# Kernel optimization log

Hardware: AMD Instinct MI355X
Metric: run time of the kernel (lower is better)

## Reference

```python
import jax, jax.numpy as jnp
import numpy as np

N = 100000   # num nodes
E = 1600000  # num edges
D = 64       # feature / hidden dim (irreps_in == hidden_dim)
SCALE = D ** -0.5


def setup_inputs() -> dict:
    key = jax.random.key(0)
    ks = jax.random.split(key, 6)
    x = jax.random.normal(ks[0], (N, D), dtype=jnp.float32)
    edge_index = jax.random.randint(ks[1], (2, E), 0, N, dtype=jnp.int32)
    std = D ** -0.5
    Wq = jax.random.normal(ks[2], (D, D), dtype=jnp.float32) * std
    Wk = jax.random.normal(ks[3], (D, D), dtype=jnp.float32) * std
    Wv = jax.random.normal(ks[4], (D, D), dtype=jnp.float32) * std
    Wo = jax.random.normal(ks[5], (D, D), dtype=jnp.float32) * std
    return {"x": x, "edge_index": edge_index, "Wq": Wq, "Wk": Wk, "Wv": Wv, "Wo": Wo}


def reference(x, edge_index, Wq, Wk, Wv, Wo):
    # Per-receiver variable-length attention over incoming neighbors.
    # Mathematically identical to the torch module's degree-bucketed SDPA
    # (softmax over each node's neighbor set), without padding buffers.
    sender, receiver = edge_index[0], edge_index[1]
    Q = x @ Wq  # [N, D]
    K = x @ Wk
    V = x @ Wv
    # per-edge logits: <Q[receiver], K[sender]> * scale
    s = jnp.einsum('ed,ed->e', Q[receiver], K[sender]) * SCALE  # [E]
    # numerically stable segment softmax over receiver groups
    m = jax.ops.segment_max(s, receiver, num_segments=N)  # -inf for empty segments
    m_safe = jnp.where(jnp.isfinite(m), m, 0.0)
    p = jnp.exp(s - m_safe[receiver])  # [E]
    denom = jax.ops.segment_sum(p, receiver, num_segments=N)  # [N]
    num = jax.ops.segment_sum(p[:, None] * V[sender], receiver, num_segments=N)  # [N, D]
    # zero-degree nodes get out = 0 (matches torch: skipped buckets + nan_to_num)
    out = jnp.where(denom[:, None] > 0,
                    num / jnp.maximum(denom, 1e-30)[:, None],
                    0.0)
    return x + out @ Wo
```

## Files before the change

kernel.cpp:

```cpp
#include <hip/hip_runtime.h>
#include <hip/hip_bf16.h>

#define DIM 64
#define SCALE 0.125f
#define BINSH 5
#define NPB 32
#define BCAP 768
#define CHUNK 8192
#define MAXBINS 3200

static __device__ __forceinline__ unsigned int pack2bf(float a, float b) {
    unsigned int ua = __float_as_uint(a), ub = __float_as_uint(b);
    ua += 0x7fffu + ((ua >> 16) & 1u);
    ub += 0x7fffu + ((ub >> 16) & 1u);
    return (ua >> 16) | (ub & 0xffff0000u);
}
static __device__ __forceinline__ float2 unpack2bf(unsigned int u) {
    return make_float2(__uint_as_float(u << 16), __uint_as_float(u & 0xffff0000u));
}

__global__ __launch_bounds__(256) void k_wmul(const float* __restrict__ Wv,
                                              const float* __restrict__ Wo,
                                              float* __restrict__ Wvo) {
    __shared__ __align__(16) float av[64 * 64];
    __shared__ __align__(16) float bo[64 * 64];
    int tid = threadIdx.x;
    for (int i = tid; i < 1024; i += 256) {
        ((float4*)av)[i] = ((const float4*)Wv)[i];
        ((float4*)bo)[i] = ((const float4*)Wo)[i];
    }
    __syncthreads();
    int r = tid >> 2, c0 = (tid & 3) * 16;
    float acc[16];
#pragma unroll
    for (int j = 0; j < 16; j++) acc[j] = 0.f;
    for (int k = 0; k < 64; k++) {
        float a = av[r * 64 + k];
#pragma unroll
        for (int j = 0; j < 16; j++)
            acc[j] = fmaf(a, bo[k * 64 + c0 + j], acc[j]);
    }
#pragma unroll
    for (int j = 0; j < 16; j++) Wvo[r * 64 + c0 + j] = acc[j];
}

__global__ __launch_bounds__(256) void k_fused(const int* __restrict__ send,
                                               const int* __restrict__ recv,
                                               const float* __restrict__ x,
                                               const float* __restrict__ Wq,
                                               const float* __restrict__ Wk,
                                               const float* __restrict__ Wvo,
                                               int* __restrict__ binCur,
                                               unsigned int* __restrict__ ebufA,
                                               float* __restrict__ Q,
                                               unsigned int* __restrict__ KVb,
                                               int E, int N, int NBK,
                                               int NBIN, int nchunk) {
    __shared__ __align__(16) float smem[16384];
    int tid = threadIdx.x;

    if ((int)blockIdx.x < NBIN) {
        int* hist = (int*)smem;
        int* lcur = hist + MAXBINS;
        int base = blockIdx.x * CHUNK;
        int lim = min(base + CHUNK, E);

        for (int i = tid; i < NBK; i += 256) hist[i] = 0;
        __syncthreads();
        for (int i = base + tid; i < lim; i += 256)
            atomicAdd(&hist[recv[i] >> BINSH], 1);
        __syncthreads();
        for (int i = tid; i < NBK; i += 256) {
            int h = hist[i];
            lcur[i] = h ? atomicAdd(&binCur[i], h) : 0;
        }
        __syncthreads();
        for (int i = base + tid; i < lim; i += 256) {
            int r = recv[i];
            int b = r >> BINSH;
            int p = atomicAdd(&lcur[b], 1);
            if (p < BCAP)
                ebufA[(size_t)b * BCAP + p] =
                    (unsigned)send[i] | ((unsigned)(r & (NPB - 1)) << 17);
        }
        return;
    }

    int wv = tid >> 6;
    int lane = tid & 63;
    int qb = blockIdx.x - NBIN;
    int m = qb / nchunk;
    int cb = qb % nchunk;
    const float* W = (m == 0) ? Wq : ((m == 1) ? Wk : Wvo);

    int base = cb * 256 + wv * 64;
    if (base < N) {
        float* xw = smem + wv * 4096;
#pragma unroll
        for (int c4 = 0; c4 < 16; c4++) {
            float4 v = make_float4(0.f, 0.f, 0.f, 0.f);
            if (base + lane < N) v = ((const float4*)x)[(size_t)(base + lane) * 16 + c4];
            xw[(c4 * 4 + 0) * 64 + lane] = v.x;
            xw[(c4 * 4 + 1) * 64 + lane] = v.y;
            xw[(c4 * 4 + 2) * 64 + lane] = v.z;
            xw[(c4 * 4 + 3) * 64 + lane] = v.w;
        }
        asm volatile("s_waitcnt lgkmcnt(0)" ::: "memory");

        int lr = lane >> 3;
        int lc = lane & 7;
        const float* xp = xw + lr * 8;
        const float* wp = W + lc * 8;

        float acc[8][8];
#pragma unroll
        for (int i = 0; i < 8; i++)
#pragma unroll
            for (int j = 0; j < 8; j++) acc[i][j] = 0.f;

        float4 xa = *(const float4*)(xp);
        float4 xb = *(const float4*)(xp + 4);
        float4 wa0 = *(const float4*)(wp);
        float4 wb0 = *(const float4*)(wp + 4);
        float4 wa1 = *(const float4*)(wp + 64);
        float4 wb1 = *(const float4*)(wp + 68);
#pragma unroll 4
        for (int k = 0; k < 64; k++) {
            float4 xan, xbn, wan, wbn;
            if (k < 63) {
                xan = *(const float4*)(xp + (k + 1) * 64);
                xbn = *(const float4*)(xp + (k + 1) * 64 + 4);
            }
            if (k < 62) {
                wan = *(const float4*)(wp + (k + 2) * 64);
                wbn = *(const float4*)(wp + (k + 2) * 64 + 4);
            }
            float xv[8] = {xa.x, xa.y, xa.z, xa.w, xb.x, xb.y, xb.z, xb.w};
            float wc[8] = {wa0.x, wa0.y, wa0.z, wa0.w, wb0.x, wb0.y, wb0.z, wb0.w};
#pragma unroll
            for (int i = 0; i < 8; i++)
#pragma unroll
                for (int j = 0; j < 8; j++)
                    acc[i][j] = fmaf(xv[i], wc[j], acc[i][j]);
            xa = xan; xb = xbn;
            wa0 = wa1; wb0 = wb1;
            wa1 = wan; wb1 = wbn;
        }

#pragma unroll
        for (int i = 0; i < 8; i++) {
            int row = base + lr * 8 + i;
            if (row < N) {
                if (m == 0) {
                    float* dst = &Q[(size_t)row * 64 + lc * 8];
                    ((float4*)dst)[0] = make_float4(acc[i][0], acc[i][1], acc[i][2], acc[i][3]);
                    ((float4*)dst)[1] = make_float4(acc[i][4], acc[i][5], acc[i][6], acc[i][7]);
                } else {
                    unsigned int* dst = &KVb[(size_t)row * 64 + (m - 1) * 32 + lc * 4];
                    uint4 pk;
                    pk.x = pack2bf(acc[i][0], acc[i][1]);
                    pk.y = pack2bf(acc[i][2], acc[i][3]);
                    pk.z = pack2bf(acc[i][4], acc[i][5]);
                    pk.w = pack2bf(acc[i][6], acc[i][7]);
                    *((uint4*)dst) = pk;
                }
            }
        }
    }
}

__global__ __launch_bounds__(256) void k_attn(const float* __restrict__ Q,
                                              const unsigned int* __restrict__ KVb,
                                              const float* __restrict__ x,
                                              const int* __restrict__ binCur,
                                              const unsigned int* __restrict__ ebufA,
                                              float* __restrict__ out, int N) {
    __shared__ unsigned int llist[BCAP];
    __shared__ int ldeg[NPB], lofs[NPB + 1], lcur[NPB];
    int tid = threadIdx.x;
    int wv = tid >> 6;
    int lane = tid & 63;
    int g = lane >> 3;
    int sub = lane & 7;

    int j = blockIdx.x;
    int cnt = min(binCur[j], BCAP);
    const unsigned int* ebin = ebufA + (size_t)j * BCAP;

    if (tid < NPB) ldeg[tid] = 0;
    __syncthreads();

    for (int i = tid; i < cnt; i += 256)
        atomicAdd(&ldeg[(ebin[i] >> 17) & (NPB - 1)], 1);
    __syncthreads();

    if (wv == 0 && lane < NPB) {
        int d = ldeg[lane];
        int s = d;
        for (int o = 1; o < NPB; o <<= 1) {
            int t = __shfl_up(s, o, NPB);
            if ((lane & (NPB - 1)) >= o) s += t;
        }
        lofs[lane + 1] = s;
        lcur[lane] = s - d;
        if (lane == 0) lofs[0] = 0;
    }
    __syncthreads();

    for (int i = tid; i < cnt; i += 256) {
        unsigned int u = ebin[i];
        int n = (u >> 17) & (NPB - 1);
        int p = atomicAdd(&lcur[n], 1);
        llist[p] = u & 0x1FFFFu;
    }
    __syncthreads();

    for (int n = wv; n < NPB; n += 4) {
        int r = (j << BINSH) + n;
        if (r >= N) break;
        int start = lofs[n];
        int end = lofs[n + 1];
        float4 qa = *((const float4*)&Q[(size_t)r * 64 + sub * 8]);
        float4 qb = *((const float4*)&Q[(size_t)r * 64 + sub * 8 + 4]);
        float q[8] = {qa.x, qa.y, qa.z, qa.w, qb.x, qb.y, qb.z, qb.w};
        float acc[8] = {0.f, 0.f, 0.f, 0.f, 0.f, 0.f, 0.f, 0.f};
        float dpart = 0.f;

        int eA = start + g;
        bool vA = eA < end;
        unsigned int sA = vA ? llist[eA] : 0u;
        uint4 kA = *((const uint4*)&KVb[(size_t)sA * 64 + sub * 4]);
        uint4 uA = *((const uint4*)&KVb[(size_t)sA * 64 + 32 + sub * 4]);
        int eB = start + 8 + g;
        bool vB = eB < end;
        unsigned int sB = vB ? llist[eB] : 0u;
        uint4 kB = *((const uint4*)&KVb[(size_t)sB * 64 + sub * 4]);
        uint4 uB = *((const uint4*)&KVb[(size_t)sB * 64 + 32 + sub * 4]);

        for (int bb = start; bb < end; bb += 8) {
            int eC = bb + 16 + g;
            bool vC = eC < end;
            unsigned int sC = vC ? llist[eC] : 0u;
            uint4 kC = *((const uint4*)&KVb[(size_t)sC * 64 + sub * 4]);
            uint4 uC = *((const uint4*)&KVb[(size_t)sC * 64 + 32 + sub * 4]);

            float2 k01 = unpack2bf(kA.x), k23 = unpack2bf(kA.y);
            float2 k45 = unpack2bf(kA.z), k67 = unpack2bf(kA.w);
            float dot = q[0] * k01.x + q[1] * k01.y + q[2] * k23.x + q[3] * k23.y
                      + q[4] * k45.x + q[5] * k45.y + q[6] * k67.x + q[7] * k67.y;
            dot += __shfl_xor(dot, 1);
            dot += __shfl_xor(dot, 2);
            dot += __shfl_xor(dot, 4);
            float w = vA ? __expf(dot * SCALE) : 0.f;

            float2 v01 = unpack2bf(uA.x), v23 = unpack2bf(uA.y);
            float2 v45 = unpack2bf(uA.z), v67 = unpack2bf(uA.w);
            acc[0] = fmaf(w, v01.x, acc[0]);
            acc[1] = fmaf(w, v01.y, acc[1]);
            acc[2] = fmaf(w, v23.x, acc[2]);
            acc[3] = fmaf(w, v23.y, acc[3]);
            acc[4] = fmaf(w, v45.x, acc[4]);
            acc[5] = fmaf(w, v45.y, acc[5]);
            acc[6] = fmaf(w, v67.x, acc[6]);
            acc[7] = fmaf(w, v67.y, acc[7]);
            dpart += w;

            kA = kB; uA = uB; vA = vB;
            kB = kC; uB = uC; vB = vC;
        }

        dpart += __shfl_xor(dpart, 8); dpart += __shfl_xor(dpart, 16); dpart += __shfl_xor(dpart, 32);
#pragma unroll
        for (int jj = 0; jj < 8; jj++) {
            acc[jj] += __shfl_xor(acc[jj], 8);
            acc[jj] += __shfl_xor(acc[jj], 16);
            acc[jj] += __shfl_xor(acc[jj], 32);
        }

        float inv = (dpart > 0.f) ? (1.0f / dpart) : 0.f;

        if (g == 0) {
            float4 xa = *((const float4*)&x[(size_t)r * 64 + sub * 8]);
            float4 xb = *((const float4*)&x[(size_t)r * 64 + sub * 8 + 4]);
            float4 oa = make_float4(fmaf(acc[0], inv, xa.x), fmaf(acc[1], inv, xa.y),
                                    fmaf(acc[2], inv, xa.z), fmaf(acc[3], inv, xa.w));
            float4 ob = make_float4(fmaf(acc[4], inv, xb.x), fmaf(acc[5], inv, xb.y),
                                    fmaf(acc[6], inv, xb.z), fmaf(acc[7], inv, xb.w));
            *((float4*)&out[(size_t)r * 64 + sub * 8]) = oa;
            *((float4*)&out[(size_t)r * 64 + sub * 8 + 4]) = ob;
        }
    }
}


extern "C" void kernel_launch(void* const* d_in, const int* in_sizes, int n_in,
                              void* d_out, int out_size, void* d_ws, size_t ws_size,
                              hipStream_t stream) {
    const float* x  = (const float*)d_in[0];
    const int* edge = (const int*)d_in[1];
    const float* Wq = (const float*)d_in[2];
    const float* Wk = (const float*)d_in[3];
    const float* Wv = (const float*)d_in[4];
    const float* Wo = (const float*)d_in[5];
    float* out = (float*)d_out;

    int N = in_sizes[0] / DIM;
    int E = in_sizes[1] / 2;
    int NBK = (N + NPB - 1) >> BINSH;

    char* p = (char*)d_ws;
    auto cv = [&](size_t bytes) {
        char* r = p;
        p += ((bytes + 255) / 256) * 256;
        return r;
    };
    float*        Q      = (float*)cv((size_t)N * 64 * 4);
    unsigned int* KVb    = (unsigned int*)cv((size_t)N * 64 * 4);
    float*        Wvo    = (float*)cv(64 * 64 * 4);
    int*          binCur = (int*)cv((size_t)NBK * 4);
    unsigned int* ebufA  = (unsigned int*)cv((size_t)NBK * BCAP * 4);
    (void)ws_size; (void)n_in; (void)out_size;

    const int* send = edge;
    const int* recv = edge + E;

    int NBIN = (E + CHUNK - 1) / CHUNK;
    int nchunk = (N + 255) / 256;

    hipMemsetAsync(binCur, 0, (size_t)NBK * 4, stream);
    k_wmul<<<1, 256, 0, stream>>>(Wv, Wo, Wvo);
    k_fused<<<NBIN + 3 * nchunk, 256, 0, stream>>>(send, recv, x, Wq, Wk, Wvo,
                                                   binCur, ebufA, Q, KVb,
                                                   E, N, NBK, NBIN, nchunk);
    k_attn<<<NBK, 256, 0, stream>>>(Q, KVb, x, binCur, ebufA, out, N);
}
```

Measured before the change: 231.1 us.

## Restructure edge binning into coarse buckets with a separate per-node CSR pass

```diff
diff --git a/kernel.cpp b/kernel.cpp
--- a/kernel.cpp
+++ b/kernel.cpp
@@ -6,8 +6,11 @@
 #define BINSH 5
 #define NPB 32
 #define BCAP 768
-#define CHUNK 8192
-#define MAXBINS 3200
+#define DBSH 8
+#define NDB 256
+#define CBCAP 4864
+#define CHUNKA 16384
+#define MAXCB 512
 
 static __device__ __forceinline__ unsigned int pack2bf(float a, float b) {
     unsigned int ua = __float_as_uint(a), ub = __float_as_uint(b);
@@ -19,98 +22,131 @@
     return make_float2(__uint_as_float(u << 16), __uint_as_float(u & 0xffff0000u));
 }
 
-__global__ __launch_bounds__(256) void k_wmul(const float* __restrict__ Wv,
-                                              const float* __restrict__ Wo,
-                                              float* __restrict__ Wvo) {
-    __shared__ __align__(16) float av[64 * 64];
-    __shared__ __align__(16) float bo[64 * 64];
+__global__ __launch_bounds__(1024) void k_prepA(const int* __restrict__ send,
+                                                const int* __restrict__ recv,
+                                                const float* __restrict__ Wv,
+                                                const float* __restrict__ Wo,
+                                                float* __restrict__ Wvo,
+                                                int* __restrict__ bucketCur,
+                                                unsigned int* __restrict__ cbuf,
+                                                int E, int NCB) {
+    __shared__ __align__(16) float smem[8192];
+    int* hist = (int*)smem;
+    int* lcur = hist + MAXCB;
     int tid = threadIdx.x;
-    for (int i = tid; i < 1024; i += 256) {
-        ((float4*)av)[i] = ((const float4*)Wv)[i];
-        ((float4*)bo)[i] = ((const float4*)Wo)[i];
-    }
-    __syncthreads();
-    int r = tid >> 2, c0 = (tid & 3) * 16;
-    float acc[16];
-#pragma unroll
-    for (int j = 0; j < 16; j++) acc[j] = 0.f;
-    for (int k = 0; k < 64; k++) {
-        float a = av[r * 64 + k];
-#pragma unroll
-        for (int j = 0; j < 16; j++)
-            acc[j] = fmaf(a, bo[k * 64 + c0 + j], acc[j]);
-    }
-#pragma unroll
-    for (int j = 0; j < 16; j++) Wvo[r * 64 + c0 + j] = acc[j];
-}
-
-__global__ __launch_bounds__(256) void k_fused(const int* __restrict__ send,
-                                               const int* __restrict__ recv,
-                                               const float* __restrict__ x,
+
+    if (blockIdx.x == 0) {
+        float* av = smem;
+        float* bo = smem + 4096;
+        ((float4*)av)[tid] = ((const float4*)Wv)[tid];
+        ((float4*)bo)[tid] = ((const float4*)Wo)[tid];
+        __syncthreads();
+        int r = tid >> 4, c0 = (tid & 15) * 4;
+        float acc[4] = {0.f, 0.f, 0.f, 0.f};
+        for (int k = 0; k < 64; k++) {
+            float a = av[r * 64 + k];
+#pragma unroll
+            for (int j = 0; j < 4; j++) acc[j] = fmaf(a, bo[k * 64 + c0 + j], acc[j]);
+        }
+#pragma unroll
+        for (int j = 0; j < 4; j++) Wvo[r * 64 + c0 + j] = acc[j];
+        __syncthreads();
+    }
+
+    int base = blockIdx.x * CHUNKA;
+    int lim = min(base + CHUNKA, E);
+
+    for (int i = tid; i < NCB; i += 1024) hist[i] = 0;
+    __syncthreads();
+    for (int i = base + tid; i < lim; i += 1024)
+        atomicAdd(&hist[recv[i] >> DBSH], 1);
+    __syncthreads();
+    for (int i = tid; i < NCB; i += 1024) {
+        int h = hist[i];
+        lcur[i] = h ? atomicAdd(&bucketCur[i], h) : 0;
+    }
+    __syncthreads();
+    for (int i = base + tid; i < lim; i += 1024) {
+        int r = recv[i];
+        int b = r >> DBSH;
+        int p = atomicAdd(&lcur[b], 1);
+        if (p < CBCAP)
+            cbuf[(size_t)b * CBCAP + p] =
+                (unsigned)send[i] | ((unsigned)(r & (NDB - 1)) << 17);
+    }
+}
+
+__global__ __launch_bounds__(256) void k_fused(const float* __restrict__ x,
                                                const float* __restrict__ Wq,
                                                const float* __restrict__ Wk,
                                                const float* __restrict__ Wvo,
-                                               int* __restrict__ binCur,
-                                               unsigned int* __restrict__ ebufA,
+                                               const int* __restrict__ bucketCur,
+                                               unsigned int* __restrict__ cbuf,
+                                               int* __restrict__ nstart,
+                                               int* __restrict__ ncount,
                                                float* __restrict__ Q,
                                                unsigned int* __restrict__ KVb,
-                                               int E, int N, int NBK,
-                                               int NBIN, int nchunk) {
-    __shared__ __align__(16) float smem[16384];
+                                               int N, int NCB, int nchunk) {
+    __shared__ __align__(16) float smem[8192];
     int tid = threadIdx.x;
-
-    if ((int)blockIdx.x < NBIN) {
-        int* hist = (int*)smem;
-        int* lcur = hist + MAXBINS;
-        int base = blockIdx.x * CHUNK;
-        int lim = min(base + CHUNK, E);
-
-        for (int i = tid; i < NBK; i += 256) hist[i] = 0;
-        __syncthreads();
-        for (int i = base + tid; i < lim; i += 256)
-            atomicAdd(&hist[recv[i] >> BINSH], 1);
-        __syncthreads();
-        for (int i = tid; i < NBK; i += 256) {
-            int h = hist[i];
-            lcur[i] = h ? atomicAdd(&binCur[i], h) : 0;
-        }
-        __syncthreads();
-        for (int i = base + tid; i < lim; i += 256) {
-            int r = recv[i];
-            int b = r >> BINSH;
-            int p = atomicAdd(&lcur[b], 1);
-            if (p < BCAP)
-                ebufA[(size_t)b * BCAP + p] =
-                    (unsigned)send[i] | ((unsigned)(r & (NPB - 1)) << 17);
-        }
-        return;
-    }
-
     int wv = tid >> 6;
     int lane = tid & 63;
-    int qb = blockIdx.x - NBIN;
+
+    if ((int)blockIdx.x < NCB) {
+        int b = blockIdx.x;
+        int bbase = b * CBCAP;
+        int cnt = min(bucketCur[b], CBCAP);
+        unsigned int* elist = (unsigned int*)smem;
+        int* ldeg = (int*)smem + CBCAP;
+        int* lcur = ldeg + NDB;
+        int* wsum = lcur + NDB;
+
+        for (int i = tid; i < cnt; i += 256) elist[i] = cbuf[bbase + i];
+        ldeg[tid] = 0;
+        __syncthreads();
+        for (int i = tid; i < cnt; i += 256)
+            atomicAdd(&ldeg[(elist[i] >> 17) & (NDB - 1)], 1);
+        __syncthreads();
+
+        int d = ldeg[tid];
+        int incl = d;
+        for (int o = 1; o < 64; o <<= 1) {
+            int t = __shfl_up(incl, o, 64);
+            if (lane >= o) incl += t;
+        }
+        if (lane == 63) wsum[wv] = incl;
+        __syncthreads();
+        int woff = 0;
+        for (int w2 = 0; w2 < wv; w2++) woff += wsum[w2];
+        int start = woff + incl - d;
+        lcur[tid] = start;
+        int r = (b << DBSH) + tid;
+        if (r < N) {
+            nstart[r] = bbase + start;
+            ncount[r] = d;
+        }
+        __syncthreads();
+
+        for (int i = tid; i < cnt; i += 256) {
+            unsigned u = elist[i];
+            int n = (u >> 17) & (NDB - 1);
+            int p = atomicAdd(&lcur[n], 1);
+            cbuf[bbase + p] = u & 0x1FFFFu;
+        }
+        return;
+    }
+
+    int qb = blockIdx.x - NCB;
     int m = qb / nchunk;
     int cb = qb % nchunk;
     const float* W = (m == 0) ? Wq : ((m == 1) ? Wk : Wvo);
 
     int base = cb * 256 + wv * 64;
     if (base < N) {
-        float* xw = smem + wv * 4096;
-#pragma unroll
-        for (int c4 = 0; c4 < 16; c4++) {
-            float4 v = make_float4(0.f, 0.f, 0.f, 0.f);
-            if (base + lane < N) v = ((const float4*)x)[(size_t)(base + lane) * 16 + c4];
-            xw[(c4 * 4 + 0) * 64 + lane] = v.x;
-            xw[(c4 * 4 + 1) * 64 + lane] = v.y;
-            xw[(c4 * 4 + 2) * 64 + lane] = v.z;
-            xw[(c4 * 4 + 3) * 64 + lane] = v.w;
-        }
-        asm volatile("s_waitcnt lgkmcnt(0)" ::: "memory");
-
+        float* xw = smem + wv * 2048;
         int lr = lane >> 3;
         int lc = lane & 7;
         const float* xp = xw + lr * 8;
-        const float* wp = W + lc * 8;
 
         float acc[8][8];
 #pragma unroll
@@ -118,33 +154,50 @@
 #pragma unroll
             for (int j = 0; j < 8; j++) acc[i][j] = 0.f;
 
-        float4 xa = *(const float4*)(xp);
-        float4 xb = *(const float4*)(xp + 4);
-        float4 wa0 = *(const float4*)(wp);
-        float4 wb0 = *(const float4*)(wp + 4);
-        float4 wa1 = *(const float4*)(wp + 64);
-        float4 wb1 = *(const float4*)(wp + 68);
+#pragma unroll
+        for (int h = 0; h < 2; h++) {
+#pragma unroll
+            for (int c4 = 0; c4 < 8; c4++) {
+                float4 v = make_float4(0.f, 0.f, 0.f, 0.f);
+                if (base + lane < N)
+                    v = ((const float4*)x)[(size_t)(base + lane) * 16 + h * 8 + c4];
+                xw[(c4 * 4 + 0) * 64 + lane] = v.x;
+                xw[(c4 * 4 + 1) * 64 + lane] = v.y;
+                xw[(c4 * 4 + 2) * 64 + lane] = v.z;
+                xw[(c4 * 4 + 3) * 64 + lane] = v.w;
+            }
+            asm volatile("s_waitcnt lgkmcnt(0)" ::: "memory");
+
+            const float* wp = W + h * 2048 + lc * 8;
+
+            float4 xa = *(const float4*)(xp);
+            float4 xb = *(const float4*)(xp + 4);
+            float4 wa0 = *(const float4*)(wp);
+            float4 wb0 = *(const float4*)(wp + 4);
+            float4 wa1 = *(const float4*)(wp + 64);
+            float4 wb1 = *(const float4*)(wp + 68);
 #pragma unroll 4
-        for (int k = 0; k < 64; k++) {
-            float4 xan, xbn, wan, wbn;
-            if (k < 63) {
-                xan = *(const float4*)(xp + (k + 1) * 64);
-                xbn = *(const float4*)(xp + (k + 1) * 64 + 4);
+            for (int kk = 0; kk < 32; kk++) {
+                float4 xan, xbn, wan, wbn;
+                if (kk < 31) {
+                    xan = *(const float4*)(xp + (kk + 1) * 64);
+                    xbn = *(const float4*)(xp + (kk + 1) * 64 + 4);
+                }
+                if (kk < 30) {
+                    wan = *(const float4*)(wp + (kk + 2) * 64);
+                    wbn = *(const float4*)(wp + (kk + 2) * 64 + 4);
+                }
+                float xv[8] = {xa.x, xa.y, xa.z, xa.w, xb.x, xb.y, xb.z, xb.w};
+                float wc[8] = {wa0.x, wa0.y, wa0.z, wa0.w, wb0.x, wb0.y, wb0.z, wb0.w};
+#pragma unroll
+                for (int i = 0; i < 8; i++)
+#pragma unroll
+                    for (int j = 0; j < 8; j++)
+                        acc[i][j] = fmaf(xv[i], wc[j], acc[i][j]);
+                xa = xan; xb = xbn;
+                wa0 = wa1; wb0 = wb1;
+                wa1 = wan; wb1 = wbn;
             }
-            if (k < 62) {
-                wan = *(const float4*)(wp + (k + 2) * 64);
-                wbn = *(const float4*)(wp + (k + 2) * 64 + 4);
-            }
-            float xv[8] = {xa.x, xa.y, xa.z, xa.w, xb.x, xb.y, xb.z, xb.w};
-            float wc[8] = {wa0.x, wa0.y, wa0.z, wa0.w, wb0.x, wb0.y, wb0.z, wb0.w};
-#pragma unroll
-            for (int i = 0; i < 8; i++)
-#pragma unroll
-                for (int j = 0; j < 8; j++)
-                    acc[i][j] = fmaf(xv[i], wc[j], acc[i][j]);
-            xa = xan; xb = xbn;
-            wa0 = wa1; wb0 = wb1;
-            wa1 = wan; wb1 = wbn;
         }
 
 #pragma unroll
@@ -172,11 +225,13 @@
 __global__ __launch_bounds__(256) void k_attn(const float* __restrict__ Q,
                                               const unsigned int* __restrict__ KVb,
                                               const float* __restrict__ x,
-                                              const int* __restrict__ binCur,
-                                              const unsigned int* __restrict__ ebufA,
+                                              const int* __restrict__ nstart,
+                                              const int* __restrict__ ncount,
+                                              const unsigned int* __restrict__ nlist,
                                               float* __restrict__ out, int N) {
     __shared__ unsigned int llist[BCAP];
-    __shared__ int ldeg[NPB], lofs[NPB + 1], lcur[NPB];
+    __shared__ int lofs[NPB + 1];
+    __shared__ int sbs;
     int tid = threadIdx.x;
     int wv = tid >> 6;
     int lane = tid & 63;
@@ -184,39 +239,24 @@
     int sub = lane & 7;
 
     int j = blockIdx.x;
-    int cnt = min(binCur[j], BCAP);
-    const unsigned int* ebin = ebufA + (size_t)j * BCAP;
-
-    if (tid < NPB) ldeg[tid] = 0;
-    __syncthreads();
-
-    for (int i = tid; i < cnt; i += 256)
-        atomicAdd(&ldeg[(ebin[i] >> 17) & (NPB - 1)], 1);
-    __syncthreads();
-
-    if (wv == 0 && lane < NPB) {
-        int d = ldeg[lane];
-        int s = d;
-        for (int o = 1; o < NPB; o <<= 1) {
-            int t = __shfl_up(s, o, NPB);
-            if ((lane & (NPB - 1)) >= o) s += t;
-        }
-        lofs[lane + 1] = s;
-        lcur[lane] = s - d;
-        if (lane == 0) lofs[0] = 0;
-    }
-    __syncthreads();
-
-    for (int i = tid; i < cnt; i += 256) {
-        unsigned int u = ebin[i];
-        int n = (u >> 17) & (NPB - 1);
-        int p = atomicAdd(&lcur[n], 1);
-        llist[p] = u & 0x1FFFFu;
-    }
+    int r0 = j << BINSH;
+
+    if (tid == 0) sbs = nstart[r0];
+    __syncthreads();
+    int sbase = sbs;
+    if (tid < NPB) {
+        int r = r0 + tid;
+        lofs[tid] = min(nstart[r] - sbase, BCAP);
+        if (tid == NPB - 1)
+            lofs[NPB] = min(nstart[r] + ncount[r] - sbase, BCAP);
+    }
+    __syncthreads();
+    int cnt = lofs[NPB];
+    for (int i = tid; i < cnt; i += 256) llist[i] = nlist[sbase + i];
     __syncthreads();
 
     for (int n = wv; n < NPB; n += 4) {
-        int r = (j << BINSH) + n;
+        int r = r0 + n;
         if (r >= N) break;
         int start = lofs[n];
         int end = lofs[n + 1];
@@ -307,6 +347,7 @@
     int N = in_sizes[0] / DIM;
     int E = in_sizes[1] / 2;
     int NBK = (N + NPB - 1) >> BINSH;
+    int NCB = (N + NDB - 1) >> DBSH;
 
     char* p = (char*)d_ws;
     auto cv = [&](size_t bytes) {
@@ -314,23 +355,25 @@
         p += ((bytes + 255) / 256) * 256;
         return r;
     };
-    float*        Q      = (float*)cv((size_t)N * 64 * 4);
-    unsigned int* KVb    = (unsigned int*)cv((size_t)N * 64 * 4);
-    float*        Wvo    = (float*)cv(64 * 64 * 4);
-    int*          binCur = (int*)cv((size_t)NBK * 4);
-    unsigned int* ebufA  = (unsigned int*)cv((size_t)NBK * BCAP * 4);
+    float*        Q         = (float*)cv((size_t)N * 64 * 4);
+    unsigned int* KVb       = (unsigned int*)cv((size_t)N * 64 * 4);
+    float*        Wvo       = (float*)cv(64 * 64 * 4);
+    int*          bucketCur = (int*)cv((size_t)NCB * 4);
+    unsigned int* cbuf      = (unsigned int*)cv((size_t)NCB * CBCAP * 4);
+    int*          nstart    = (int*)cv((size_t)N * 4);
+    int*          ncount    = (int*)cv((size_t)N * 4);
     (void)ws_size; (void)n_in; (void)out_size;
 
     const int* send = edge;
     const int* recv = edge + E;
 
-    int NBIN = (E + CHUNK - 1) / CHUNK;
+    int NBA = (E + CHUNKA - 1) / CHUNKA;
     int nchunk = (N + 255) / 256;
 
-    hipMemsetAsync(binCur, 0, (size_t)NBK * 4, stream);
-    k_wmul<<<1, 256, 0, stream>>>(Wv, Wo, Wvo);
-    k_fused<<<NBIN + 3 * nchunk, 256, 0, stream>>>(send, recv, x, Wq, Wk, Wvo,
-                                                   binCur, ebufA, Q, KVb,
-                                                   E, N, NBK, NBIN, nchunk);
-    k_attn<<<NBK, 256, 0, stream>>>(Q, KVb, x, binCur, ebufA, out, N);
-}
+    hipMemsetAsync(bucketCur, 0, (size_t)NCB * 4, stream);
+    k_prepA<<<NBA, 1024, 0, stream>>>(send, recv, Wv, Wo, Wvo, bucketCur, cbuf, E, NCB);
+    k_fused<<<NCB + 3 * nchunk, 256, 0, stream>>>(x, Wq, Wk, Wvo, bucketCur, cbuf,
+                                                  nstart, ncount, Q, KVb,
+                                                  N, NCB, nchunk);
+    k_attn<<<NBK, 256, 0, stream>>>(Q, KVb, x, nstart, ncount, cbuf, out, N);
+}
```

Result: slower. 236.4 us (+2.3%).
